# Kernel tuning notes

Hardware: AMD Instinct MI355X
Metric: run time of the kernel (lower is better)

The kernel has to match this reference:

```python
import jax, jax.numpy as jnp
import numpy as np

VOCAB, DIM = 100000, 300
B, L = 4096, 200
HIDDEN, OUT = 1000, 3


def setup_inputs() -> dict:
    key = jax.random.key(0)
    k_emb, k_x, k_len, k_w1, k_b1, k_w2, k_b2 = jax.random.split(key, 7)
    emb_table = jax.random.normal(k_emb, (VOCAB, DIM), dtype=jnp.float32)
    x = jax.random.randint(k_x, (B, L), 0, VOCAB)
    lengths = jax.random.randint(k_len, (B,), 1, L + 1)  # >=1 to avoid div-by-zero
    W1 = jax.random.normal(k_w1, (2 * DIM, HIDDEN), dtype=jnp.float32) * 0.02
    b1 = jax.random.normal(k_b1, (HIDDEN,), dtype=jnp.float32) * 0.02
    W2 = jax.random.normal(k_w2, (HIDDEN, OUT), dtype=jnp.float32) * 0.02
    b2 = jax.random.normal(k_b2, (OUT,), dtype=jnp.float32) * 0.02
    return {"emb_table": emb_table, "W1": W1, "b1": b1, "W2": W2, "b2": b2,
            "x": x, "lengths": lengths}


def reference(emb_table, W1, b1, W2, b2, x, lengths):
    emb = emb_table[x]                                   # [B, L, D] gather
    # Faithful to original: mean uses sum over ALL positions (incl. padding)
    mean_pooled = jnp.sum(emb, axis=1) / lengths[:, None].astype(emb.dtype)  # [B, D]
    # Max only over the first `length` real tokens
    mask = jnp.arange(L)[None, :] < lengths[:, None]     # [B, L]
    neg_inf = jnp.array(-jnp.inf, dtype=emb.dtype)
    max_pooled = jnp.max(jnp.where(mask[:, :, None], emb, neg_inf), axis=1)  # [B, D]
    rep = jnp.concatenate([mean_pooled, max_pooled], axis=1)  # [B, 2D]
    h = jax.nn.relu(rep @ W1 + b1)                       # [B, 1000]
    return h @ W2 + b2                                   # [B, OUT]
```

## Files before the change

### kernel.cpp

```cpp
#include <hip/hip_runtime.h>
#include <math.h>

#define VOCAB  100000
#define DIM    300
#define IDIM   320
#define BB     4096
#define LL     200
#define HIDDEN 1000
#define OUTC   3
#define KT     19
#define NT     64
#define MTILES (BB / 16)

#define QSCALE (6.0f / 127.0f)
#define QINV   (127.0f / 6.0f)

typedef __attribute__((ext_vector_type(8))) short  short8;
typedef __attribute__((ext_vector_type(4))) float  floatx4;

__device__ inline ushort f2bf(float f) {
    union { float f; unsigned u; } v; v.f = f;
    unsigned u = v.u;
    u += 0x7fffu + ((u >> 16) & 1u);
    return (ushort)(u >> 16);
}
__device__ inline float4 f4max(float4 a, float4 b) {
    return make_float4(fmaxf(a.x, b.x), fmaxf(a.y, b.y), fmaxf(a.z, b.z), fmaxf(a.w, b.w));
}
__device__ inline float4 f4add(float4 a, float4 b) {
    return make_float4(a.x + b.x, a.y + b.y, a.z + b.z, a.w + b.w);
}

__device__ inline int a_slot(int k, int ml) {
    const int kt = k >> 5, kk = k & 31;
    return ((kt << 6) + ml + ((kk >> 3) << 4)) * 8 + (kk & 7);
}

__global__ __launch_bounds__(256) void init_out(const float* __restrict__ b2,
                                                float* __restrict__ out) {
    const int g = blockIdx.x * 256 + threadIdx.x;
    if (g < BB * OUTC) out[g] = b2[g % OUTC];
}

__device__ inline unsigned q4(float a, float b, float c, float d) {
    int q0 = min(max(__float2int_rn(a * QINV) + 128, 0), 255);
    int q1 = min(max(__float2int_rn(b * QINV) + 128, 0), 255);
    int q2 = min(max(__float2int_rn(c * QINV) + 128, 0), 255);
    int q3 = min(max(__float2int_rn(d * QINV) + 128, 0), 255);
    return (unsigned)q0 | ((unsigned)q1 << 8) | ((unsigned)q2 << 16) | ((unsigned)q3 << 24);
}

__global__ __launch_bounds__(256) void conv_emb_i8(const float* __restrict__ emb,
                                                   unsigned char* __restrict__ embQ) {
    const int g = blockIdx.x * 256 + threadIdx.x;
    if (g >= VOCAB * 20) return;
    const int row = g / 20;
    const int c   = g - row * 20;
    const float4* rp = (const float4*)(emb + (size_t)row * DIM);
    uint4 o;
    unsigned* ow = (unsigned*)&o;
    #pragma unroll
    for (int v = 0; v < 4; ++v) {
        const int fi = 4 * c + v;
        float4 f = (fi < 75) ? rp[fi] : make_float4(0.f, 0.f, 0.f, 0.f);
        ow[v] = q4(f.x, f.y, f.z, f.w);
    }
    *(uint4*)(embQ + (size_t)g * 16) = o;
}

__global__ __launch_bounds__(256) void prep_w1(const float* __restrict__ W1,
                                               ushort* __restrict__ w1p) {
    const int g = blockIdx.x * 256 + threadIdx.x;
    if (g >= KT * NT * 64) return;
    const int lane = g & 63;
    const int nt   = (g >> 6) & (NT - 1);
    const int kt   = g >> 12;
    const int n    = nt * 16 + (lane & 15);
    const int kb   = kt * 32 + ((lane >> 4) << 3);
    short8 v;
    #pragma unroll
    for (int j = 0; j < 8; ++j) {
        const int k = kb + j;
        const float f = (k < 600 && n < HIDDEN) ? W1[k * HIDDEN + n] : 0.f;
        v[j] = (short)f2bf(f);
    }
    ((short8*)w1p)[g] = v;
}

__global__ __launch_bounds__(256, 8) void gather_pool_i8(
    const unsigned char* __restrict__ embQ,
    const int*           __restrict__ x,
    const int*           __restrict__ lengths,
    ushort*              __restrict__ repA)
{
    __shared__ int   xS[LL];
    __shared__ float pS[3][20][16];
    __shared__ float pM[3][20][16];

    const int tid  = threadIdx.x;
    const int lane = tid & 63;
    const int wave = tid >> 6;
    const int row  = blockIdx.x;

    for (int i = tid; i < LL; i += 256) xS[i] = x[row * LL + i];
    const int len = lengths[row];
    __syncthreads();

    const int  t0   = wave * 50;
    const int  vmax = min(max(len - t0, 0), 50);
    const bool ga   = (lane < 20);
    const bool ld   = (lane < 40);
    const int  lg   = ga ? lane : (lane - 20);

    float s[16], m[16];
    #pragma unroll
    for (int j = 0; j < 16; ++j) { s[j] = 0.f; m[j] = -INFINITY; }

    uint4 raw = make_uint4(0, 0, 0, 0);
    const int full = vmax >> 1;
    int p = 0;
    for (; p < full; ++p) {
        const int tA  = t0 + 2 * p;
        const int idx = ga ? xS[tA] : xS[tA + 1];
        if (ld) raw = *(const uint4*)(embQ + (size_t)idx * IDIM + 16 * lg);
        const unsigned* ww = (const unsigned*)&raw;
        #pragma unroll
        for (int w = 0; w < 4; ++w) {
            const unsigned u = ww[w];
            const float f0 = (float)(u & 0xff);
            const float f1 = (float)((u >> 8) & 0xff);
            const float f2 = (float)((u >> 16) & 0xff);
            const float f3 = (float)(u >> 24);
            s[4*w+0] += f0; m[4*w+0] = fmaxf(m[4*w+0], f0);
            s[4*w+1] += f1; m[4*w+1] = fmaxf(m[4*w+1], f1);
            s[4*w+2] += f2; m[4*w+2] = fmaxf(m[4*w+2], f2);
            s[4*w+3] += f3; m[4*w+3] = fmaxf(m[4*w+3], f3);
        }
    }
    if (vmax & 1) {
        const int tA  = t0 + 2 * p;
        const int idx = ga ? xS[tA] : xS[tA + 1];
        if (ld) raw = *(const uint4*)(embQ + (size_t)idx * IDIM + 16 * lg);
        const unsigned* ww = (const unsigned*)&raw;
        #pragma unroll
        for (int w = 0; w < 4; ++w) {
            const unsigned u = ww[w];
            const float f0 = (float)(u & 0xff);
            const float f1 = (float)((u >> 8) & 0xff);
            const float f2 = (float)((u >> 16) & 0xff);
            const float f3 = (float)(u >> 24);
            s[4*w+0] += f0; m[4*w+0] = ga ? fmaxf(m[4*w+0], f0) : m[4*w+0];
            s[4*w+1] += f1; m[4*w+1] = ga ? fmaxf(m[4*w+1], f1) : m[4*w+1];
            s[4*w+2] += f2; m[4*w+2] = ga ? fmaxf(m[4*w+2], f2) : m[4*w+2];
            s[4*w+3] += f3; m[4*w+3] = ga ? fmaxf(m[4*w+3], f3) : m[4*w+3];
        }
        ++p;
    }
    for (; p < 25; ++p) {
        const int tA  = t0 + 2 * p;
        const int idx = ga ? xS[tA] : xS[tA + 1];
        if (ld) raw = *(const uint4*)(embQ + (size_t)idx * IDIM + 16 * lg);
        const unsigned* ww = (const unsigned*)&raw;
        #pragma unroll
        for (int w = 0; w < 4; ++w) {
            const unsigned u = ww[w];
            s[4*w+0] += (float)(u & 0xff);
            s[4*w+1] += (float)((u >> 8) & 0xff);
            s[4*w+2] += (float)((u >> 16) & 0xff);
            s[4*w+3] += (float)(u >> 24);
        }
    }

    {
        const int src = ga ? (lane + 20) : lane;
        #pragma unroll
        for (int j = 0; j < 16; ++j) {
            s[j] += __shfl(s[j], src);
            m[j] = fmaxf(m[j], __shfl(m[j], src));
        }
    }

    if (wave != 0 && ga) {
        #pragma unroll
        for (int j = 0; j < 16; ++j) { pS[wave-1][lane][j] = s[j]; pM[wave-1][lane][j] = m[j]; }
    }
    __syncthreads();
    if (wave == 0 && ga) {
        #pragma unroll
        for (int w = 0; w < 3; ++w)
            #pragma unroll
            for (int j = 0; j < 16; ++j) {
                s[j] += pS[w][lane][j];
                m[j] = fmaxf(m[j], pM[w][lane][j]);
            }

        const float c1 = QSCALE / (float)len;
        const int mt = row >> 4;
        const int ml = row & 15;
        ushort* rb = repA + (size_t)mt * (KT * 512);

        ushort mv[16];
        #pragma unroll
        for (int j = 0; j < 16; ++j) mv[j] = f2bf((m[j] - 128.f) * QSCALE);

        if (lane < 18) {
            #pragma unroll
            for (int h = 0; h < 2; ++h) {
                short8 q;
                #pragma unroll
                for (int j = 0; j < 8; ++j)
                    q[j] = (short)f2bf((s[8*h + j] - 25600.f) * c1);
                *(short8*)(rb + a_slot(16 * lane + 8 * h, ml)) = q;
            }
            #pragma unroll
            for (int h = 0; h < 2; ++h) {
                const int k0 = 300 + 16 * lane + 8 * h;
                *(ushort4*)(rb + a_slot(k0, ml)) =
                    make_ushort4(mv[8*h+0], mv[8*h+1], mv[8*h+2], mv[8*h+3]);
                *(ushort4*)(rb + a_slot(k0 + 4, ml)) =
                    make_ushort4(mv[8*h+4], mv[8*h+5], mv[8*h+6], mv[8*h+7]);
            }
        } else if (lane == 18) {
            short8 q;
            #pragma unroll
            for (int j = 0; j < 8; ++j) q[j] = (short)f2bf((s[j] - 25600.f) * c1);
            *(short8*)(rb + a_slot(288, ml)) = q;
            *(ushort4*)(rb + a_slot(296, ml)) =
                make_ushort4(f2bf((s[8] - 25600.f) * c1), f2bf((s[9] - 25600.f) * c1),
                             f2bf((s[10] - 25600.f) * c1), f2bf((s[11] - 25600.f) * c1));
            *(ushort4*)(rb + a_slot(588, ml)) = make_ushort4(mv[0], mv[1], mv[2], mv[3]);
            *(ushort4*)(rb + a_slot(592, ml)) = make_ushort4(mv[4], mv[5], mv[6], mv[7]);
            *(ushort4*)(rb + a_slot(596, ml)) = make_ushort4(mv[8], mv[9], mv[10], mv[11]);
            *(ushort4*)(rb + a_slot(600, ml)) = make_ushort4(0, 0, 0, 0);
        } else {
            *(ushort4*)(rb + a_slot(604, ml)) = make_ushort4(0, 0, 0, 0);
        }
    }
}

__global__ __launch_bounds__(256, 8) void gather_pool_f32(
    const float* __restrict__ emb,
    const int*   __restrict__ x,
    const int*   __restrict__ lengths,
    ushort*      __restrict__ repA)
{
    __shared__ int    xS[LL];
    __shared__ float4 pS[3][75];
    __shared__ float4 pM[3][75];

    const int tid  = threadIdx.x;
    const int lane = tid & 63;
    const int wave = tid >> 6;
    const int row  = blockIdx.x;

    for (int i = tid; i < LL; i += 256) xS[i] = x[row * LL + i];
    const int len = lengths[row];
    __syncthreads();

    const int  t0   = wave * (LL / 4);
    const int  vmax = min(max(len - t0, 0), LL / 4);
    const bool tl   = (lane < 11);
    const float4 z4 = make_float4(0.f, 0.f, 0.f, 0.f);

    float4 s4 = z4, st = z4;
    float4 m4 = make_float4(-INFINITY, -INFINITY, -INFINITY, -INFINITY);
    float4 mt = m4;

    int t = 0;
    #pragma unroll 4
    for (; t < vmax; ++t) {
        const int idx = xS[t0 + t];
        const float4* rp = (const float4*)(emb + (size_t)idx * DIM);
        float4 a = rp[lane];
        float4 b = tl ? rp[64 + lane] : z4;
        s4 = f4add(s4, a); st = f4add(st, b);
        m4 = f4max(m4, a); mt = f4max(mt, b);
    }
    #pragma unroll 4
    for (; t < LL / 4; ++t) {
        const int idx = xS[t0 + t];
        const float4* rp = (const float4*)(emb + (size_t)idx * DIM);
        float4 a = rp[lane];
        float4 b = tl ? rp[64 + lane] : z4;
        s4 = f4add(s4, a); st = f4add(st, b);
    }

    if (wave != 0) {
        pS[wave - 1][lane] = s4; pM[wave - 1][lane] = m4;
        if (tl) { pS[wave - 1][64 + lane] = st; pM[wave - 1][64 + lane] = mt; }
    }
    __syncthreads();
    if (wave == 0) {
        #pragma unroll
        for (int w = 0; w < 3; ++w) {
            s4 = f4add(s4, pS[w][lane]); m4 = f4max(m4, pM[w][lane]);
            if (tl) { st = f4add(st, pS[w][64 + lane]); mt = f4max(mt, pM[w][64 + lane]); }
        }
        const float inv = 1.0f / (float)len;
        const int mtile = row >> 4;
        const int ml    = row & 15;
        ushort* rb = repA + (size_t)mtile * (KT * 512);
        {
            ushort4 q = make_ushort4(f2bf(s4.x*inv), f2bf(s4.y*inv), f2bf(s4.z*inv), f2bf(s4.w*inv));
            *(ushort4*)(rb + a_slot(4 * lane, ml)) = q;
        }
        {
            ushort4 q = make_ushort4(f2bf(m4.x), f2bf(m4.y), f2bf(m4.z), f2bf(m4.w));
            *(ushort4*)(rb + a_slot(300 + 4 * lane, ml)) = q;
        }
        if (tl) {
            ushort4 q1 = make_ushort4(f2bf(st.x*inv), f2bf(st.y*inv), f2bf(st.z*inv), f2bf(st.w*inv));
            *(ushort4*)(rb + a_slot(256 + 4 * lane, ml)) = q1;
            ushort4 q2 = make_ushort4(f2bf(mt.x), f2bf(mt.y), f2bf(mt.z), f2bf(mt.w));
            *(ushort4*)(rb + a_slot(556 + 4 * lane, ml)) = q2;
        }
        if (lane >= 56) rb[a_slot(600 + (lane - 56), ml)] = 0;
    }
}

__global__ __launch_bounds__(256, 4) void mlp_mfma(
    const ushort* __restrict__ w1p,
    const ushort* __restrict__ repA,
    const float*  __restrict__ b1,
    const float*  __restrict__ W2,
    float*        __restrict__ out)
{
    __shared__ float red[4][16][3];

    const int tid  = threadIdx.x;
    const int lane = tid & 63;
    const int wave = tid >> 6;
    const int mt   = blockIdx.x >> 2;
    const int q    = blockIdx.x & 3;

    short8 a[KT];
    const short8* ap = (const short8*)(repA + (size_t)mt * (KT * 512));
    #pragma unroll
    for (int kt = 0; kt < KT; ++kt) a[kt] = ap[kt * 64 + lane];

    float po[4][3];
    #pragma unroll
    for (int rg = 0; rg < 4; ++rg)
        #pragma unroll
        for (int j = 0; j < OUTC; ++j) po[rg][j] = 0.f;

    const short8* bp = (const short8*)w1p;

    #pragma unroll
    for (int p = 0; p < 2; ++p) {
        const int nt0 = q * 16 + wave * 4 + 2 * p;
        const int nt1 = nt0 + 1;
        floatx4 acc0 = {0.f, 0.f, 0.f, 0.f};
        floatx4 acc1 = {0.f, 0.f, 0.f, 0.f};
        #pragma unroll
        for (int kt = 0; kt < KT; ++kt) {
            short8 bf0 = bp[(kt * NT + nt0) * 64 + lane];
            short8 bf1 = bp[(kt * NT + nt1) * 64 + lane];
            acc0 = __builtin_amdgcn_mfma_f32_16x16x32_bf16(a[kt], bf0, acc0, 0, 0, 0);
            acc1 = __builtin_amdgcn_mfma_f32_16x16x32_bf16(a[kt], bf1, acc1, 0, 0, 0);
        }
        #pragma unroll
        for (int s = 0; s < 2; ++s) {
            const floatx4 acc = s ? acc1 : acc0;
            const int n = (s ? nt1 : nt0) * 16 + (lane & 15);
            const bool valid = (n < HIDDEN);
            const float bb  = b1[valid ? n : 0];
            const float w20 = valid ? W2[n * 3 + 0] : 0.f;
            const float w21 = valid ? W2[n * 3 + 1] : 0.f;
            const float w22 = valid ? W2[n * 3 + 2] : 0.f;
            #pragma unroll
            for (int rg = 0; rg < 4; ++rg) {
                const float h = fmaxf(acc[rg] + bb, 0.f);
                po[rg][0] = fmaf(h, w20, po[rg][0]);
                po[rg][1] = fmaf(h, w21, po[rg][1]);
                po[rg][2] = fmaf(h, w22, po[rg][2]);
            }
        }
    }

    #pragma unroll
    for (int rg = 0; rg < 4; ++rg) {
        #pragma unroll
        for (int j = 0; j < OUTC; ++j) {
            float v = po[rg][j];
            v += __shfl_xor(v, 1);
            v += __shfl_xor(v, 2);
            v += __shfl_xor(v, 4);
            v += __shfl_xor(v, 8);
            if ((lane & 15) == 0) red[wave][(lane >> 4) * 4 + rg][j] = v;
        }
    }
    __syncthreads();

    if (tid < 16 * OUTC) {
        const int m = tid / OUTC, j = tid % OUTC;
        const float s = red[0][m][j] + red[1][m][j] + red[2][m][j] + red[3][m][j];
        atomicAdd(&out[(size_t)(mt * 16 + m) * OUTC + j], s);
    }
}

extern "C" void kernel_launch(void* const* d_in, const int* in_sizes, int n_in,
                              void* d_out, int out_size, void* d_ws, size_t ws_size,
                              hipStream_t stream) {
    const float* emb = (const float*)d_in[0];
    const float* W1  = (const float*)d_in[1];
    const float* b1  = (const float*)d_in[2];
    const float* W2  = (const float*)d_in[3];
    const float* b2  = (const float*)d_in[4];
    const int*   x   = (const int*)d_in[5];
    const int*   len = (const int*)d_in[6];
    float* out = (float*)d_out;

    const size_t W1P_ELTS  = (size_t)KT * NT * 64 * 8;
    const size_t REPA_ELTS = (size_t)MTILES * KT * 512;
    ushort* w1p  = (ushort*)d_ws;
    ushort* repA = w1p + W1P_ELTS;
    unsigned char* embQ = (unsigned char*)(repA + REPA_ELTS);
    const size_t need = (W1P_ELTS + REPA_ELTS) * 2 + (size_t)VOCAB * IDIM;

    hipLaunchKernelGGL(init_out, dim3((BB * OUTC + 255) / 256), dim3(256), 0, stream,
                       b2, out);
    hipLaunchKernelGGL(prep_w1, dim3((KT * NT * 64 + 255) / 256), dim3(256), 0, stream,
                       W1, w1p);
    if (ws_size >= need) {
        hipLaunchKernelGGL(conv_emb_i8, dim3((VOCAB * 20 + 255) / 256), dim3(256), 0, stream,
                           emb, embQ);
        hipLaunchKernelGGL(gather_pool_i8, dim3(BB), dim3(256), 0, stream,
                           embQ, x, len, repA);
    } else {
        hipLaunchKernelGGL(gather_pool_f32, dim3(BB), dim3(256), 0, stream,
                           emb, x, len, repA);
    }
    hipLaunchKernelGGL(mlp_mfma, dim3(MTILES * 4), dim3(256), 0, stream,
                       w1p, repA, b1, W2, out);
}
```

Measured before the change: 272.7 us.

## Merge prep kernels, use packed integer pooling, stage MLP A tiles in LDS

Three separate changes. The three prep kernels (W1 repack, output init, embedding quantisation) become one launch with block ranges, removing two launch gaps. The int8 gather-pool now accumulates sums and maxima as packed 16-bit lanes in 32-bit integers, replacing per-byte float conversion and fmax work in the inner loop. The MLP kernel stages the A tile once in shared memory and computes four N tiles per wave in a single K loop, which cuts register pressure from holding 19 A fragments but adds an LDS pass and a barrier.

```diff
diff --git a/kernel.cpp b/kernel.cpp
--- a/kernel.cpp
+++ b/kernel.cpp
@@ -15,8 +15,13 @@
 #define QSCALE (6.0f / 127.0f)
 #define QINV   (127.0f / 6.0f)
 
+#define W1_BLKS   ((KT * NT * 64 + 255) / 256)
+#define INIT_BLKS ((BB * OUTC + 255) / 256)
+#define CONV_BLKS ((VOCAB * 20 + 255) / 256)
+
 typedef __attribute__((ext_vector_type(8))) short  short8;
 typedef __attribute__((ext_vector_type(4))) float  floatx4;
+typedef __attribute__((ext_vector_type(2))) unsigned short ushort2v;
 
 __device__ inline ushort f2bf(float f) {
     union { float f; unsigned u; } v; v.f = f;
@@ -30,16 +35,16 @@
 __device__ inline float4 f4add(float4 a, float4 b) {
     return make_float4(a.x + b.x, a.y + b.y, a.z + b.z, a.w + b.w);
 }
+__device__ inline unsigned pkmax16(unsigned a, unsigned b) {
+    union { unsigned u; ushort2v v; } x, y, r;
+    x.u = a; y.u = b;
+    r.v = __builtin_elementwise_max(x.v, y.v);
+    return r.u;
+}
 
 __device__ inline int a_slot(int k, int ml) {
     const int kt = k >> 5, kk = k & 31;
     return ((kt << 6) + ml + ((kk >> 3) << 4)) * 8 + (kk & 7);
-}
-
-__global__ __launch_bounds__(256) void init_out(const float* __restrict__ b2,
-                                                float* __restrict__ out) {
-    const int g = blockIdx.x * 256 + threadIdx.x;
-    if (g < BB * OUTC) out[g] = b2[g % OUTC];
 }
 
 __device__ inline unsigned q4(float a, float b, float c, float d) {
@@ -50,41 +55,48 @@
     return (unsigned)q0 | ((unsigned)q1 << 8) | ((unsigned)q2 << 16) | ((unsigned)q3 << 24);
 }
 
-__global__ __launch_bounds__(256) void conv_emb_i8(const float* __restrict__ emb,
-                                                   unsigned char* __restrict__ embQ) {
-    const int g = blockIdx.x * 256 + threadIdx.x;
-    if (g >= VOCAB * 20) return;
-    const int row = g / 20;
-    const int c   = g - row * 20;
-    const float4* rp = (const float4*)(emb + (size_t)row * DIM);
-    uint4 o;
-    unsigned* ow = (unsigned*)&o;
-    #pragma unroll
-    for (int v = 0; v < 4; ++v) {
-        const int fi = 4 * c + v;
-        float4 f = (fi < 75) ? rp[fi] : make_float4(0.f, 0.f, 0.f, 0.f);
-        ow[v] = q4(f.x, f.y, f.z, f.w);
-    }
-    *(uint4*)(embQ + (size_t)g * 16) = o;
-}
-
-__global__ __launch_bounds__(256) void prep_w1(const float* __restrict__ W1,
-                                               ushort* __restrict__ w1p) {
-    const int g = blockIdx.x * 256 + threadIdx.x;
-    if (g >= KT * NT * 64) return;
-    const int lane = g & 63;
-    const int nt   = (g >> 6) & (NT - 1);
-    const int kt   = g >> 12;
-    const int n    = nt * 16 + (lane & 15);
-    const int kb   = kt * 32 + ((lane >> 4) << 3);
-    short8 v;
-    #pragma unroll
-    for (int j = 0; j < 8; ++j) {
-        const int k = kb + j;
-        const float f = (k < 600 && n < HIDDEN) ? W1[k * HIDDEN + n] : 0.f;
-        v[j] = (short)f2bf(f);
-    }
-    ((short8*)w1p)[g] = v;
+__global__ __launch_bounds__(256) void prep_all(
+    const float* __restrict__ emb, unsigned char* __restrict__ embQ,
+    const float* __restrict__ W1,  ushort* __restrict__ w1p,
+    const float* __restrict__ b2,  float* __restrict__ out)
+{
+    const int bid = blockIdx.x;
+    const int tid = threadIdx.x;
+    if (bid < W1_BLKS) {
+        const int g = bid * 256 + tid;
+        if (g >= KT * NT * 64) return;
+        const int lane = g & 63;
+        const int nt   = (g >> 6) & (NT - 1);
+        const int kt   = g >> 12;
+        const int n    = nt * 16 + (lane & 15);
+        const int kb   = kt * 32 + ((lane >> 4) << 3);
+        short8 v;
+        #pragma unroll
+        for (int j = 0; j < 8; ++j) {
+            const int k = kb + j;
+            const float f = (k < 600 && n < HIDDEN) ? W1[k * HIDDEN + n] : 0.f;
+            v[j] = (short)f2bf(f);
+        }
+        ((short8*)w1p)[g] = v;
+    } else if (bid < W1_BLKS + INIT_BLKS) {
+        const int g = (bid - W1_BLKS) * 256 + tid;
+        if (g < BB * OUTC) out[g] = b2[g % OUTC];
+    } else {
+        const int g = (bid - W1_BLKS - INIT_BLKS) * 256 + tid;
+        if (g >= VOCAB * 20) return;
+        const int row = g / 20;
+        const int c   = g - row * 20;
+        const float4* rp = (const float4*)(emb + (size_t)row * DIM);
+        uint4 o;
+        unsigned* ow = (unsigned*)&o;
+        #pragma unroll
+        for (int v = 0; v < 4; ++v) {
+            const int fi = 4 * c + v;
+            float4 f = (fi < 75) ? rp[fi] : make_float4(0.f, 0.f, 0.f, 0.f);
+            ow[v] = q4(f.x, f.y, f.z, f.w);
+        }
+        *(uint4*)(embQ + (size_t)g * 16) = o;
+    }
 }
 
 __global__ __launch_bounds__(256, 8) void gather_pool_i8(
@@ -93,9 +105,9 @@
     const int*           __restrict__ lengths,
     ushort*              __restrict__ repA)
 {
-    __shared__ int   xS[LL];
-    __shared__ float pS[3][20][16];
-    __shared__ float pM[3][20][16];
+    __shared__ int      xS[LL];
+    __shared__ unsigned pS[3][20][8];
+    __shared__ unsigned pM[3][20][8];
 
     const int tid  = threadIdx.x;
     const int lane = tid & 63;
@@ -112,9 +124,9 @@
     const bool ld   = (lane < 40);
     const int  lg   = ga ? lane : (lane - 20);
 
-    float s[16], m[16];
-    #pragma unroll
-    for (int j = 0; j < 16; ++j) { s[j] = 0.f; m[j] = -INFINITY; }
+    unsigned sLo[4], sHi[4], mLo[4], mHi[4];
+    #pragma unroll
+    for (int w = 0; w < 4; ++w) { sLo[w] = sHi[w] = 0u; mLo[w] = mHi[w] = 0u; }
 
     uint4 raw = make_uint4(0, 0, 0, 0);
     const int full = vmax >> 1;
@@ -126,15 +138,12 @@
         const unsigned* ww = (const unsigned*)&raw;
         #pragma unroll
         for (int w = 0; w < 4; ++w) {
-            const unsigned u = ww[w];
-            const float f0 = (float)(u & 0xff);
-            const float f1 = (float)((u >> 8) & 0xff);
-            const float f2 = (float)((u >> 16) & 0xff);
-            const float f3 = (float)(u >> 24);
-            s[4*w+0] += f0; m[4*w+0] = fmaxf(m[4*w+0], f0);
-            s[4*w+1] += f1; m[4*w+1] = fmaxf(m[4*w+1], f1);
-            s[4*w+2] += f2; m[4*w+2] = fmaxf(m[4*w+2], f2);
-            s[4*w+3] += f3; m[4*w+3] = fmaxf(m[4*w+3], f3);
+            const unsigned u  = ww[w];
+            const unsigned lo = u & 0x00FF00FFu;
+            const unsigned hi = (u >> 8) & 0x00FF00FFu;
+            sLo[w] += lo;  sHi[w] += hi;
+            mLo[w] = pkmax16(mLo[w], lo);
+            mHi[w] = pkmax16(mHi[w], hi);
         }
     }
     if (vmax & 1) {
@@ -144,15 +153,14 @@
         const unsigned* ww = (const unsigned*)&raw;
         #pragma unroll
         for (int w = 0; w < 4; ++w) {
-            const unsigned u = ww[w];
-            const float f0 = (float)(u & 0xff);
-            const float f1 = (float)((u >> 8) & 0xff);
-            const float f2 = (float)((u >> 16) & 0xff);
-            const float f3 = (float)(u >> 24);
-            s[4*w+0] += f0; m[4*w+0] = ga ? fmaxf(m[4*w+0], f0) : m[4*w+0];
-            s[4*w+1] += f1; m[4*w+1] = ga ? fmaxf(m[4*w+1], f1) : m[4*w+1];
-            s[4*w+2] += f2; m[4*w+2] = ga ? fmaxf(m[4*w+2], f2) : m[4*w+2];
-            s[4*w+3] += f3; m[4*w+3] = ga ? fmaxf(m[4*w+3], f3) : m[4*w+3];
+            const unsigned u  = ww[w];
+            const unsigned lo = u & 0x00FF00FFu;
+            const unsigned hi = (u >> 8) & 0x00FF00FFu;
+            sLo[w] += lo;  sHi[w] += hi;
+            if (ga) {
+                mLo[w] = pkmax16(mLo[w], lo);
+                mHi[w] = pkmax16(mHi[w], hi);
+            }
         }
         ++p;
     }
@@ -164,35 +172,55 @@
         #pragma unroll
         for (int w = 0; w < 4; ++w) {
             const unsigned u = ww[w];
-            s[4*w+0] += (float)(u & 0xff);
-            s[4*w+1] += (float)((u >> 8) & 0xff);
-            s[4*w+2] += (float)((u >> 16) & 0xff);
-            s[4*w+3] += (float)(u >> 24);
+            sLo[w] += u & 0x00FF00FFu;
+            sHi[w] += (u >> 8) & 0x00FF00FFu;
         }
     }
 
     {
         const int src = ga ? (lane + 20) : lane;
         #pragma unroll
-        for (int j = 0; j < 16; ++j) {
-            s[j] += __shfl(s[j], src);
-            m[j] = fmaxf(m[j], __shfl(m[j], src));
+        for (int w = 0; w < 4; ++w) {
+            sLo[w] += (unsigned)__shfl((int)sLo[w], src);
+            sHi[w] += (unsigned)__shfl((int)sHi[w], src);
+            mLo[w] = pkmax16(mLo[w], (unsigned)__shfl((int)mLo[w], src));
+            mHi[w] = pkmax16(mHi[w], (unsigned)__shfl((int)mHi[w], src));
         }
     }
 
     if (wave != 0 && ga) {
         #pragma unroll
-        for (int j = 0; j < 16; ++j) { pS[wave-1][lane][j] = s[j]; pM[wave-1][lane][j] = m[j]; }
+        for (int w = 0; w < 4; ++w) {
+            pS[wave - 1][lane][w]     = sLo[w];
+            pS[wave - 1][lane][4 + w] = sHi[w];
+            pM[wave - 1][lane][w]     = mLo[w];
+            pM[wave - 1][lane][4 + w] = mHi[w];
+        }
     }
     __syncthreads();
     if (wave == 0 && ga) {
         #pragma unroll
-        for (int w = 0; w < 3; ++w)
+        for (int wv = 0; wv < 3; ++wv)
             #pragma unroll
-            for (int j = 0; j < 16; ++j) {
-                s[j] += pS[w][lane][j];
-                m[j] = fmaxf(m[j], pM[w][lane][j]);
+            for (int w = 0; w < 4; ++w) {
+                sLo[w] += pS[wv][lane][w];
+                sHi[w] += pS[wv][lane][4 + w];
+                mLo[w] = pkmax16(mLo[w], pM[wv][lane][w]);
+                mHi[w] = pkmax16(mHi[w], pM[wv][lane][4 + w]);
             }
+
+        float s[16], m[16];
+        #pragma unroll
+        for (int w = 0; w < 4; ++w) {
+            s[4*w+0] = (float)(sLo[w] & 0xFFFFu);
+            s[4*w+2] = (float)(sLo[w] >> 16);
+            s[4*w+1] = (float)(sHi[w] & 0xFFFFu);
+            s[4*w+3] = (float)(sHi[w] >> 16);
+            m[4*w+0] = (float)(mLo[w] & 0xFFFFu);
+            m[4*w+2] = (float)(mLo[w] >> 16);
+            m[4*w+1] = (float)(mHi[w] & 0xFFFFu);
+            m[4*w+3] = (float)(mHi[w] >> 16);
+        }
 
         const float c1 = QSCALE / (float)len;
         const int mt = row >> 4;
@@ -325,7 +353,8 @@
     const float*  __restrict__ W2,
     float*        __restrict__ out)
 {
-    __shared__ float red[4][16][3];
+    __shared__ short8 aS[KT * 64];
+    __shared__ float  red[4][16][3];
 
     const int tid  = threadIdx.x;
     const int lane = tid & 63;
@@ -333,10 +362,31 @@
     const int mt   = blockIdx.x >> 2;
     const int q    = blockIdx.x & 3;
 
-    short8 a[KT];
-    const short8* ap = (const short8*)(repA + (size_t)mt * (KT * 512));
-    #pragma unroll
-    for (int kt = 0; kt < KT; ++kt) a[kt] = ap[kt * 64 + lane];
+    {
+        const short8* ap = (const short8*)(repA + (size_t)mt * (KT * 512));
+        for (int i = tid; i < KT * 64; i += 256) aS[i] = ap[i];
+    }
+    __syncthreads();
+
+    const int nt0 = q * 16 + wave * 4;
+    const short8* bp = (const short8*)w1p;
+
+    floatx4 acc[4];
+    #pragma unroll
+    for (int s = 0; s < 4; ++s) acc[s] = (floatx4){0.f, 0.f, 0.f, 0.f};
+
+    #pragma unroll
+    for (int kt = 0; kt < KT; ++kt) {
+        const short8 av = aS[kt * 64 + lane];
+        const short8 b0 = bp[(kt * NT + nt0 + 0) * 64 + lane];
+        const short8 b1v = bp[(kt * NT + nt0 + 1) * 64 + lane];
+        const short8 b2v = bp[(kt * NT + nt0 + 2) * 64 + lane];
+        const short8 b3 = bp[(kt * NT + nt0 + 3) * 64 + lane];
+        acc[0] = __builtin_amdgcn_mfma_f32_16x16x32_bf16(av, b0,  acc[0], 0, 0, 0);
+        acc[1] = __builtin_amdgcn_mfma_f32_16x16x32_bf16(av, b1v, acc[1], 0, 0, 0);
+        acc[2] = __builtin_amdgcn_mfma_f32_16x16x32_bf16(av, b2v, acc[2], 0, 0, 0);
+        acc[3] = __builtin_amdgcn_mfma_f32_16x16x32_bf16(av, b3,  acc[3], 0, 0, 0);
+    }
 
     float po[4][3];
     #pragma unroll
@@ -344,37 +394,20 @@
         #pragma unroll
         for (int j = 0; j < OUTC; ++j) po[rg][j] = 0.f;
 
-    const short8* bp = (const short8*)w1p;
-
-    #pragma unroll
-    for (int p = 0; p < 2; ++p) {
-        const int nt0 = q * 16 + wave * 4 + 2 * p;
-        const int nt1 = nt0 + 1;
-        floatx4 acc0 = {0.f, 0.f, 0.f, 0.f};
-        floatx4 acc1 = {0.f, 0.f, 0.f, 0.f};
-        #pragma unroll
-        for (int kt = 0; kt < KT; ++kt) {
-            short8 bf0 = bp[(kt * NT + nt0) * 64 + lane];
-            short8 bf1 = bp[(kt * NT + nt1) * 64 + lane];
-            acc0 = __builtin_amdgcn_mfma_f32_16x16x32_bf16(a[kt], bf0, acc0, 0, 0, 0);
-            acc1 = __builtin_amdgcn_mfma_f32_16x16x32_bf16(a[kt], bf1, acc1, 0, 0, 0);
-        }
-        #pragma unroll
-        for (int s = 0; s < 2; ++s) {
-            const floatx4 acc = s ? acc1 : acc0;
-            const int n = (s ? nt1 : nt0) * 16 + (lane & 15);
-            const bool valid = (n < HIDDEN);
-            const float bb  = b1[valid ? n : 0];
-            const float w20 = valid ? W2[n * 3 + 0] : 0.f;
-            const float w21 = valid ? W2[n * 3 + 1] : 0.f;
-            const float w22 = valid ? W2[n * 3 + 2] : 0.f;
-            #pragma unroll
-            for (int rg = 0; rg < 4; ++rg) {
-                const float h = fmaxf(acc[rg] + bb, 0.f);
-                po[rg][0] = fmaf(h, w20, po[rg][0]);
-                po[rg][1] = fmaf(h, w21, po[rg][1]);
-                po[rg][2] = fmaf(h, w22, po[rg][2]);
-            }
+    #pragma unroll
+    for (int s = 0; s < 4; ++s) {
+        const int n = (nt0 + s) * 16 + (lane & 15);
+        const bool valid = (n < HIDDEN);
+        const float bb  = b1[valid ? n : 0];
+        const float w20 = valid ? W2[n * 3 + 0] : 0.f;
+        const float w21 = valid ? W2[n * 3 + 1] : 0.f;
+        const float w22 = valid ? W2[n * 3 + 2] : 0.f;
+        #pragma unroll
+        for (int rg = 0; rg < 4; ++rg) {
+            const float h = fmaxf(acc[s][rg] + bb, 0.f);
+            po[rg][0] = fmaf(h, w20, po[rg][0]);
+            po[rg][1] = fmaf(h, w21, po[rg][1]);
+            po[rg][2] = fmaf(h, w22, po[rg][2]);
         }
     }
 
@@ -417,14 +450,12 @@
     ushort* repA = w1p + W1P_ELTS;
     unsigned char* embQ = (unsigned char*)(repA + REPA_ELTS);
     const size_t need = (W1P_ELTS + REPA_ELTS) * 2 + (size_t)VOCAB * IDIM;
-
-    hipLaunchKernelGGL(init_out, dim3((BB * OUTC + 255) / 256), dim3(256), 0, stream,
-                       b2, out);
-    hipLaunchKernelGGL(prep_w1, dim3((KT * NT * 64 + 255) / 256), dim3(256), 0, stream,
-                       W1, w1p);
-    if (ws_size >= need) {
-        hipLaunchKernelGGL(conv_emb_i8, dim3((VOCAB * 20 + 255) / 256), dim3(256), 0, stream,
-                           emb, embQ);
+    const bool doConv = (ws_size >= need);
+
+    const int prepGrid = W1_BLKS + INIT_BLKS + (doConv ? CONV_BLKS : 0);
+    hipLaunchKernelGGL(prep_all, dim3(prepGrid), dim3(256), 0, stream,
+                       emb, embQ, W1, w1p, b2, out);
+    if (doConv) {
         hipLaunchKernelGGL(gather_pool_i8, dim3(BB), dim3(256), 0, stream,
                            embQ, x, len, repA);
     } else {
```

Result: faster. 256.0 us (-6.1%).
